# Optimization experiments

Measured on AMD Instinct MI355X. Metric: run time of the kernel, lower is better.

## Reference

```python
import jax, jax.numpy as jnp
import numpy as np

# ---- static module config (HashEncoder defaults) ----
INPUT_DIM = 3
NUM_LEVELS = 16
LEVEL_DIM = 2
PER_LEVEL_SCALE = 2.0
BASE_RES = 16
LOG2_HASHMAP = 19
MAX_PARAMS = 2 ** LOG2_HASHMAP
S = np.log2(PER_LEVEL_SCALE)  # log2 of per-level scale, as in the CUDA kernel
B_POINTS = 1048576

# per-level table offsets, exactly as in HashEncoder.__init__
_offs = [0]
_off = 0
for _i in range(NUM_LEVELS):
    _res = int(np.ceil(BASE_RES * PER_LEVEL_SCALE ** _i))
    _p = min(MAX_PARAMS, (_res + 1) ** INPUT_DIM)
    _p = int(_p / 8) * 8
    _off += _p
    _offs.append(_off)
OFFSETS = np.array(_offs, dtype=np.int64)
N_ENTRIES = _off  # 7132272

# spatial hash primes from torch-ngp fast_hash (first 3 dims)
PRIMES = np.array([1, 2654435761, 805459861], dtype=np.uint32)


def _encode_level(inputs, emb_level, level, hashmap_size):
    """One resolution level: hash 8 corners, gather, trilinear-interp. inputs: [B,3] in [0,1]."""
    scale = np.float32(np.exp2(level * S) * BASE_RES - 1.0)
    resolution = int(np.ceil(scale)) + 1
    pos = inputs * scale + 0.5
    pos_grid = jnp.floor(pos)
    frac = pos - pos_grid                    # [B,3] trilinear fractions
    pg = pos_grid.astype(jnp.uint32)         # [B,3] base corner
    # kernel hashes whenever the dense grid would exceed the (rounded) table size
    use_hash = (resolution + 1) ** INPUT_DIM > hashmap_size
    hs = np.uint32(hashmap_size)
    out = jnp.zeros((inputs.shape[0], LEVEL_DIM), dtype=inputs.dtype)
    for c in range(2 ** INPUT_DIM):          # 8 corners
        bits = np.array([(c >> d) & 1 for d in range(INPUT_DIM)], dtype=np.uint32)
        w = jnp.prod(jnp.where(bits.astype(bool), frac, 1.0 - frac), axis=-1)  # [B]
        corner = pg + bits                   # [B,3] uint32
        if use_hash:
            h = corner * PRIMES              # uint32 wrap-around multiply
            idx = h[:, 0] ^ h[:, 1] ^ h[:, 2]
        else:
            stride = np.uint32(resolution + 1)
            idx = corner[:, 0] + corner[:, 1] * stride + corner[:, 2] * (stride * stride)
        idx = (idx % hs).astype(jnp.int32)
        out = out + w[:, None] * emb_level[idx]  # irregular gather [B,C]
    return out


def setup_inputs() -> dict:
    key = jax.random.key(0)
    k1, k2 = jax.random.split(key)
    xyz = jax.random.uniform(k1, (B_POINTS, INPUT_DIM), dtype=jnp.float32)
    # reset_parameters: uniform(-1e-4, 1e-4)
    embeddings = jax.random.uniform(k2, (N_ENTRIES, LEVEL_DIM), dtype=jnp.float32,
                                    minval=-1e-4, maxval=1e-4)
    return {"xyz": xyz, "embeddings": embeddings, "normalize": 0}


def reference(xyz, embeddings, normalize):
    # normalize == 0 -> use raw coords (kernel expects [0,1]^3), matching normalize=False path
    inputs = xyz.reshape(-1, INPUT_DIM)
    outs = []
    for l in range(NUM_LEVELS):
        o0, o1 = int(OFFSETS[l]), int(OFFSETS[l + 1])
        outs.append(_encode_level(inputs, embeddings[o0:o1], l, o1 - o0))
    # equivalent to outputs.permute(1,0,2).reshape(B, L*C)
    return jnp.concatenate(outs, axis=-1)
```

## Files before the change

### kernel.cpp

```cpp
#include <hip/hip_runtime.h>

#define NLEVELS 16
#define BLOCK 256
#define PPT 2

struct HashParams {
    unsigned offs[NLEVELS + 1];
    unsigned hsize[NLEVELS];
    unsigned hash_bits;
    unsigned pow2_bits;
};

__global__ void __launch_bounds__(BLOCK)
hashenc_pass1(const float* __restrict__ xyz,
              const float* __restrict__ emb,
              float2* __restrict__ ws,
              HashParams p, int np, int bpl_shift)
{
    const int l = blockIdx.x >> bpl_shift;
    const int chunk = blockIdx.x & ((1 << bpl_shift) - 1);
    const int tid = threadIdx.x;

    const unsigned hs = p.hsize[l];
    const float2* __restrict__ tab = (const float2*)emb + p.offs[l];
    const float scale = (float)((16u << l) - 1u);
    const bool do_hash = (p.hash_bits >> l) & 1u;
    const bool is_pow2 = (p.pow2_bits >> l) & 1u;
    float2* __restrict__ wl = ws + (size_t)l * np;

    const int base = chunk * (BLOCK * PPT) + tid;

#pragma unroll
    for (int s = 0; s < PPT; ++s) {
        const int pidx = base + s * BLOCK;
        const float x = xyz[pidx * 3 + 0];
        const float y = xyz[pidx * 3 + 1];
        const float z = xyz[pidx * 3 + 2];

        const float px = x * scale + 0.5f;
        const float py = y * scale + 0.5f;
        const float pz = z * scale + 0.5f;
        const float gx = floorf(px), gy = floorf(py), gz = floorf(pz);
        const float fx = px - gx, fy = py - gy, fz = pz - gz;
        const unsigned ix = (unsigned)gx, iy = (unsigned)gy, iz = (unsigned)gz;

        unsigned idx[8];
        if (do_hash) {
            const unsigned hy0 = iy * 2654435761u;
            const unsigned hz0 = iz * 805459861u;
            const unsigned hy1 = hy0 + 2654435761u;
            const unsigned hz1 = hz0 + 805459861u;
            if (is_pow2) {
                const unsigned m = hs - 1u;
#pragma unroll
                for (int c = 0; c < 8; ++c)
                    idx[c] = ((ix + (c & 1)) ^ ((c & 2) ? hy1 : hy0) ^ ((c & 4) ? hz1 : hz0)) & m;
            } else {
#pragma unroll
                for (int c = 0; c < 8; ++c)
                    idx[c] = ((ix + (c & 1)) ^ ((c & 2) ? hy1 : hy0) ^ ((c & 4) ? hz1 : hz0)) % hs;
            }
        } else {
            const unsigned stride = (16u << l) + 1u;
#pragma unroll
            for (int c = 0; c < 8; ++c) {
                const unsigned lin = (ix + (c & 1))
                                   + (iy + ((c >> 1) & 1)) * stride
                                   + (iz + ((c >> 2) & 1)) * stride * stride;
                idx[c] = lin % hs;
            }
        }

        float2 e[8];
#pragma unroll
        for (int c = 0; c < 8; ++c) e[c] = tab[idx[c]];

        const float wx[2] = {1.0f - fx, fx};
        const float wy[2] = {1.0f - fy, fy};
        const float wz[2] = {1.0f - fz, fz};
        float o0 = 0.0f, o1 = 0.0f;
#pragma unroll
        for (int c = 0; c < 8; ++c) {
            const float w = wx[c & 1] * wy[(c >> 1) & 1] * wz[(c >> 2) & 1];
            o0 = fmaf(w, e[c].x, o0);
            o1 = fmaf(w, e[c].y, o1);
        }
        wl[pidx] = make_float2(o0, o1);
    }
}

__global__ void __launch_bounds__(BLOCK)
hashenc_pass2(const float2* __restrict__ ws, float* __restrict__ out, int np)
{
    __shared__ float lds[BLOCK * 33];
    const int tid = threadIdx.x;
    const int p0 = blockIdx.x * BLOCK;

#pragma unroll
    for (int l = 0; l < NLEVELS; ++l) {
        const float2 v = ws[(size_t)l * np + p0 + tid];
        lds[tid * 33 + 2 * l + 0] = v.x;
        lds[tid * 33 + 2 * l + 1] = v.y;
    }
    __syncthreads();
    float* __restrict__ ochunk = out + (size_t)blockIdx.x * (BLOCK * 32);
#pragma unroll
    for (int k = 0; k < 32; ++k) {
        const int flat = k * BLOCK + tid;
        const float v = lds[(flat >> 5) * 33 + (flat & 31)];
        __builtin_nontemporal_store(v, ochunk + flat);
    }
}

__global__ void __launch_bounds__(BLOCK)
hashenc_fwd(const float* __restrict__ xyz,
            const float* __restrict__ emb,
            float* __restrict__ out,
            HashParams p)
{
    const int tid = threadIdx.x;
    const long b = (long)blockIdx.x * BLOCK + tid;
    __shared__ float lds[BLOCK * 33];

    const float x = xyz[b * 3 + 0];
    const float y = xyz[b * 3 + 1];
    const float z = xyz[b * 3 + 2];

#pragma unroll
    for (int l = 0; l < NLEVELS; ++l) {
        const float scale = (float)((16u << l) - 1u);
        const float px = x * scale + 0.5f;
        const float py = y * scale + 0.5f;
        const float pz = z * scale + 0.5f;
        const float gx = floorf(px), gy = floorf(py), gz = floorf(pz);
        const float fx = px - gx, fy = py - gy, fz = pz - gz;
        const unsigned ix = (unsigned)gx, iy = (unsigned)gy, iz = (unsigned)gz;
        const unsigned hs = p.hsize[l];
        const float2* __restrict__ tab = (const float2*)emb + p.offs[l];

        unsigned idx[8];
        if ((p.hash_bits >> l) & 1u) {
            const unsigned hy0 = iy * 2654435761u;
            const unsigned hz0 = iz * 805459861u;
            const unsigned hy1 = hy0 + 2654435761u;
            const unsigned hz1 = hz0 + 805459861u;
            if ((p.pow2_bits >> l) & 1u) {
                const unsigned m = hs - 1u;
#pragma unroll
                for (int c = 0; c < 8; ++c)
                    idx[c] = ((ix + (c & 1)) ^ ((c & 2) ? hy1 : hy0) ^ ((c & 4) ? hz1 : hz0)) & m;
            } else {
#pragma unroll
                for (int c = 0; c < 8; ++c)
                    idx[c] = ((ix + (c & 1)) ^ ((c & 2) ? hy1 : hy0) ^ ((c & 4) ? hz1 : hz0)) % hs;
            }
        } else {
            const unsigned stride = (16u << l) + 1u;
#pragma unroll
            for (int c = 0; c < 8; ++c) {
                const unsigned lin = (ix + (c & 1))
                                   + (iy + ((c >> 1) & 1)) * stride
                                   + (iz + ((c >> 2) & 1)) * stride * stride;
                idx[c] = lin % hs;
            }
        }

        float2 e[8];
#pragma unroll
        for (int c = 0; c < 8; ++c) e[c] = tab[idx[c]];

        const float wx[2] = {1.0f - fx, fx};
        const float wy[2] = {1.0f - fy, fy};
        const float wz[2] = {1.0f - fz, fz};
        float o0 = 0.0f, o1 = 0.0f;
#pragma unroll
        for (int c = 0; c < 8; ++c) {
            const float w = wx[c & 1] * wy[(c >> 1) & 1] * wz[(c >> 2) & 1];
            o0 = fmaf(w, e[c].x, o0);
            o1 = fmaf(w, e[c].y, o1);
        }
        lds[tid * 33 + l * 2 + 0] = o0;
        lds[tid * 33 + l * 2 + 1] = o1;
    }

    __syncthreads();
    float* __restrict__ ochunk = out + (long)blockIdx.x * (BLOCK * 32);
#pragma unroll
    for (int k = 0; k < 32; ++k) {
        const int flat = k * BLOCK + tid;
        const float v = lds[(flat >> 5) * 33 + (flat & 31)];
        __builtin_nontemporal_store(v, ochunk + flat);
    }
}

extern "C" void kernel_launch(void* const* d_in, const int* in_sizes, int n_in,
                              void* d_out, int out_size, void* d_ws, size_t ws_size,
                              hipStream_t stream) {
    const float* xyz = (const float*)d_in[0];
    const float* emb = (const float*)d_in[1];
    float* out = (float*)d_out;
    const int B = in_sizes[0] / 3;

    HashParams p;
    p.offs[0] = 0;
    unsigned hash_bits = 0, pow2_bits = 0;
    long off = 0;
    for (int i = 0; i < NLEVELS; ++i) {
        const long res = 16L << i;
        const long dense = (res + 1) * (res + 1) * (res + 1);
        long t = dense < (1L << 19) ? dense : (1L << 19);
        t = (t / 8) * 8;
        p.hsize[i] = (unsigned)t;
        off += t;
        p.offs[i + 1] = (unsigned)off;
        if (dense > t) hash_bits |= (1u << i);
        if ((t & (t - 1)) == 0) pow2_bits |= (1u << i);
    }
    p.hash_bits = hash_bits;
    p.pow2_bits = pow2_bits;

    const size_t need = (size_t)B * NLEVELS * sizeof(float2);
    if (ws_size >= need && (B % (BLOCK * PPT)) == 0 && (B % BLOCK) == 0) {
        int bpl_shift = 0;
        while ((1 << bpl_shift) * (BLOCK * PPT) < B) ++bpl_shift;
        const int bpl = 1 << bpl_shift;
        hashenc_pass1<<<dim3(NLEVELS * bpl), dim3(BLOCK), 0, stream>>>(
            xyz, emb, (float2*)d_ws, p, B, bpl_shift);
        hashenc_pass2<<<dim3(B / BLOCK), dim3(BLOCK), 0, stream>>>(
            (const float2*)d_ws, out, B);
    } else {
        hashenc_fwd<<<dim3(B / BLOCK), dim3(BLOCK), 0, stream>>>(xyz, emb, out, p);
    }
}
```

Before: 594.3 us.

## Pair x-adjacent hash corners into float4 loads and block workspace layout

For power-of-two hashed levels, an even ix means the two x-neighbour corners hash to adjacent entries (index differs only in bit 0). The pass-1 kernel then fetches both with one 16-byte aligned load and swaps the halves by parity, cutting gather instructions from 8 to 4 for roughly half the points. The workspace is also reorganised into 256-point chunks holding all levels contiguously, so pass 2 reads one contiguous region per block. This adds branch divergence between the paired and unpaired paths inside each wavefront.

```diff
diff --git a/kernel.cpp b/kernel.cpp
--- a/kernel.cpp
+++ b/kernel.cpp
@@ -26,7 +26,6 @@
     const float scale = (float)((16u << l) - 1u);
     const bool do_hash = (p.hash_bits >> l) & 1u;
     const bool is_pow2 = (p.pow2_bits >> l) & 1u;
-    float2* __restrict__ wl = ws + (size_t)l * np;
 
     const int base = chunk * (BLOCK * PPT) + tid;
 
@@ -44,48 +43,86 @@
         const float fx = px - gx, fy = py - gy, fz = pz - gz;
         const unsigned ix = (unsigned)gx, iy = (unsigned)gy, iz = (unsigned)gz;
 
-        unsigned idx[8];
-        if (do_hash) {
+        const float wxv[2] = {1.0f - fx, fx};
+        const float wyv[2] = {1.0f - fy, fy};
+        const float wzv[2] = {1.0f - fz, fz};
+        float o0 = 0.0f, o1 = 0.0f;
+
+        if (do_hash && is_pow2) {
+            const unsigned m = hs - 1u;
             const unsigned hy0 = iy * 2654435761u;
             const unsigned hz0 = iz * 805459861u;
             const unsigned hy1 = hy0 + 2654435761u;
             const unsigned hz1 = hz0 + 805459861u;
-            if (is_pow2) {
-                const unsigned m = hs - 1u;
-#pragma unroll
-                for (int c = 0; c < 8; ++c)
-                    idx[c] = ((ix + (c & 1)) ^ ((c & 2) ? hy1 : hy0) ^ ((c & 4) ? hz1 : hz0)) & m;
+            const unsigned hyz[4] = { hy0 ^ hz0, hy1 ^ hz0, hy0 ^ hz1, hy1 ^ hz1 };
+
+            if (!(ix & 1u)) {
+                float4 pr[4];
+                unsigned vv[4];
+#pragma unroll
+                for (int q = 0; q < 4; ++q) {
+                    vv[q] = (ix ^ hyz[q]) & m;
+                    pr[q] = *reinterpret_cast<const float4*>(tab + (vv[q] & ~1u));
+                }
+#pragma unroll
+                for (int q = 0; q < 4; ++q) {
+                    const bool sw = (vv[q] & 1u) != 0u;
+                    const float ex0x = sw ? pr[q].z : pr[q].x;
+                    const float ex0y = sw ? pr[q].w : pr[q].y;
+                    const float ex1x = sw ? pr[q].x : pr[q].z;
+                    const float ex1y = sw ? pr[q].y : pr[q].w;
+                    const float w0 = wxv[0] * wyv[q & 1] * wzv[(q >> 1) & 1];
+                    const float w1 = wxv[1] * wyv[q & 1] * wzv[(q >> 1) & 1];
+                    o0 = fmaf(w0, ex0x, o0); o1 = fmaf(w0, ex0y, o1);
+                    o0 = fmaf(w1, ex1x, o0); o1 = fmaf(w1, ex1y, o1);
+                }
             } else {
+                float2 e0[4], e1[4];
+#pragma unroll
+                for (int q = 0; q < 4; ++q) {
+                    e0[q] = tab[(ix ^ hyz[q]) & m];
+                    e1[q] = tab[((ix + 1u) ^ hyz[q]) & m];
+                }
+#pragma unroll
+                for (int q = 0; q < 4; ++q) {
+                    const float w0 = wxv[0] * wyv[q & 1] * wzv[(q >> 1) & 1];
+                    const float w1 = wxv[1] * wyv[q & 1] * wzv[(q >> 1) & 1];
+                    o0 = fmaf(w0, e0[q].x, o0); o1 = fmaf(w0, e0[q].y, o1);
+                    o0 = fmaf(w1, e1[q].x, o0); o1 = fmaf(w1, e1[q].y, o1);
+                }
+            }
+        } else {
+            unsigned idx[8];
+            if (do_hash) {
+                const unsigned hy0 = iy * 2654435761u;
+                const unsigned hz0 = iz * 805459861u;
+                const unsigned hy1 = hy0 + 2654435761u;
+                const unsigned hz1 = hz0 + 805459861u;
 #pragma unroll
                 for (int c = 0; c < 8; ++c)
                     idx[c] = ((ix + (c & 1)) ^ ((c & 2) ? hy1 : hy0) ^ ((c & 4) ? hz1 : hz0)) % hs;
-            }
-        } else {
-            const unsigned stride = (16u << l) + 1u;
+            } else {
+                const unsigned stride = (16u << l) + 1u;
+#pragma unroll
+                for (int c = 0; c < 8; ++c) {
+                    const unsigned lin = (ix + (c & 1))
+                                       + (iy + ((c >> 1) & 1)) * stride
+                                       + (iz + ((c >> 2) & 1)) * stride * stride;
+                    idx[c] = lin % hs;
+                }
+            }
+            float2 e[8];
+#pragma unroll
+            for (int c = 0; c < 8; ++c) e[c] = tab[idx[c]];
 #pragma unroll
             for (int c = 0; c < 8; ++c) {
-                const unsigned lin = (ix + (c & 1))
-                                   + (iy + ((c >> 1) & 1)) * stride
-                                   + (iz + ((c >> 2) & 1)) * stride * stride;
-                idx[c] = lin % hs;
+                const float w = wxv[c & 1] * wyv[(c >> 1) & 1] * wzv[(c >> 2) & 1];
+                o0 = fmaf(w, e[c].x, o0);
+                o1 = fmaf(w, e[c].y, o1);
             }
         }
 
-        float2 e[8];
-#pragma unroll
-        for (int c = 0; c < 8; ++c) e[c] = tab[idx[c]];
-
-        const float wx[2] = {1.0f - fx, fx};
-        const float wy[2] = {1.0f - fy, fy};
-        const float wz[2] = {1.0f - fz, fz};
-        float o0 = 0.0f, o1 = 0.0f;
-#pragma unroll
-        for (int c = 0; c < 8; ++c) {
-            const float w = wx[c & 1] * wy[(c >> 1) & 1] * wz[(c >> 2) & 1];
-            o0 = fmaf(w, e[c].x, o0);
-            o1 = fmaf(w, e[c].y, o1);
-        }
-        wl[pidx] = make_float2(o0, o1);
+        ws[((size_t)(pidx >> 8) * NLEVELS + l) * 256 + (pidx & 255)] = make_float2(o0, o1);
     }
 }
 
@@ -94,11 +131,11 @@
 {
     __shared__ float lds[BLOCK * 33];
     const int tid = threadIdx.x;
-    const int p0 = blockIdx.x * BLOCK;
+    const float2* __restrict__ chunk = ws + (size_t)blockIdx.x * (NLEVELS * 256);
 
 #pragma unroll
     for (int l = 0; l < NLEVELS; ++l) {
-        const float2 v = ws[(size_t)l * np + p0 + tid];
+        const float2 v = chunk[l * 256 + tid];
         lds[tid * 33 + 2 * l + 0] = v.x;
         lds[tid * 33 + 2 * l + 1] = v.y;
     }
@@ -220,13 +257,13 @@
     p.pow2_bits = pow2_bits;
 
     const size_t need = (size_t)B * NLEVELS * sizeof(float2);
-    if (ws_size >= need && (B % (BLOCK * PPT)) == 0 && (B % BLOCK) == 0) {
+    if (ws_size >= need && (B % (BLOCK * PPT)) == 0 && (B % 256) == 0) {
         int bpl_shift = 0;
         while ((1 << bpl_shift) * (BLOCK * PPT) < B) ++bpl_shift;
         const int bpl = 1 << bpl_shift;
         hashenc_pass1<<<dim3(NLEVELS * bpl), dim3(BLOCK), 0, stream>>>(
             xyz, emb, (float2*)d_ws, p, B, bpl_shift);
-        hashenc_pass2<<<dim3(B / BLOCK), dim3(BLOCK), 0, stream>>>(
+        hashenc_pass2<<<dim3(B / 256), dim3(BLOCK), 0, stream>>>(
             (const float2*)d_ws, out, B);
     } else {
         hashenc_fwd<<<dim3(B / BLOCK), dim3(BLOCK), 0, stream>>>(xyz, emb, out, p);
```

Measured after the change: 572.5 us. 3.7% less time.

## Convert embedding table to fp16 and pair x-neighbour corner gathers

Applied to the files above, without the earlier changes.

Each call first runs a conversion kernel that packs the float32 embedding table into half2 entries in workspace. The per-level pass then gathers these 4-byte entries, and when the x coordinate is even it fetches the two x-neighbour corners with a single 8-byte load, choosing their order from the low bit of the hash. The dense levels drop the modulo in favour of a conditional subtract, and xyz is staged through LDS with float4 loads. The aim is to halve gather bytes and gather count; the cost is an extra pass over the table every call and fp16 rounding of the embeddings.

```diff
diff --git a/kernel.cpp b/kernel.cpp
--- a/kernel.cpp
+++ b/kernel.cpp
@@ -1,4 +1,5 @@
 #include <hip/hip_runtime.h>
+#include <hip/hip_fp16.h>
 
 #define NLEVELS 16
 #define BLOCK 256
@@ -12,14 +13,147 @@
 };
 
 __global__ void __launch_bounds__(BLOCK)
-hashenc_pass1(const float* __restrict__ xyz,
-              const float* __restrict__ emb,
-              float2* __restrict__ ws,
-              HashParams p, int np, int bpl_shift)
+hashenc_conv(const float4* __restrict__ emb2, uint2* __restrict__ tab16, int n2)
+{
+    const int i = blockIdx.x * BLOCK + threadIdx.x;
+    if (i < n2) {
+        const float4 v = emb2[i];
+        const __half2 a = __floats2half2_rn(v.x, v.y);
+        const __half2 b = __floats2half2_rn(v.z, v.w);
+        tab16[i] = make_uint2(*(const unsigned*)&a, *(const unsigned*)&b);
+    }
+}
+
+__global__ void __launch_bounds__(BLOCK)
+hashenc_pass1_h(const float* __restrict__ xyz,
+                const unsigned* __restrict__ tab16,
+                float2* __restrict__ ws,
+                HashParams p, int np, int bpl_shift)
 {
     const int l = blockIdx.x >> bpl_shift;
     const int chunk = blockIdx.x & ((1 << bpl_shift) - 1);
     const int tid = threadIdx.x;
+
+    __shared__ float sxyz[BLOCK * PPT * 3];
+    {
+        const float4* __restrict__ src =
+            (const float4*)(xyz + (size_t)chunk * (BLOCK * PPT) * 3);
+        float4* __restrict__ dst = (float4*)sxyz;
+#pragma unroll
+        for (int i = tid; i < (BLOCK * PPT * 3) / 4; i += BLOCK)
+            dst[i] = src[i];
+    }
+    __syncthreads();
+
+    const unsigned hs = p.hsize[l];
+    const unsigned* __restrict__ tab = tab16 + p.offs[l];
+    const float scale = (float)((16u << l) - 1u);
+    const bool do_hash = (p.hash_bits >> l) & 1u;
+    float2* __restrict__ wl = ws + (size_t)l * np;
+
+    unsigned raw[PPT][8];
+    unsigned selba[PPT];
+    float fxa[PPT], fya[PPT], fza[PPT];
+
+#pragma unroll
+    for (int s = 0; s < PPT; ++s) {
+        const int lp = s * BLOCK + tid;
+        const float x = sxyz[lp * 3 + 0];
+        const float y = sxyz[lp * 3 + 1];
+        const float z = sxyz[lp * 3 + 2];
+        const float px = x * scale + 0.5f;
+        const float py = y * scale + 0.5f;
+        const float pz = z * scale + 0.5f;
+        const float gx = floorf(px), gy = floorf(py), gz = floorf(pz);
+        fxa[s] = px - gx; fya[s] = py - gy; fza[s] = pz - gz;
+        const unsigned ix = (unsigned)gx, iy = (unsigned)gy, iz = (unsigned)gz;
+
+        unsigned selb = 0u;
+        if (do_hash) {
+            const unsigned m = hs - 1u;
+            const unsigned hy0 = iy * 2654435761u;
+            const unsigned hz0 = iz * 805459861u;
+            const unsigned hy1 = hy0 + 2654435761u;
+            const unsigned hz1 = hz0 + 805459861u;
+            const unsigned hyz[4] = { hy0 ^ hz0, hy1 ^ hz0, hy0 ^ hz1, hy1 ^ hz1 };
+            if (!(ix & 1u)) {
+#pragma unroll
+                for (int q = 0; q < 4; ++q) {
+                    const unsigned v0 = (ix ^ hyz[q]) & m;
+                    const uint2 pr = *reinterpret_cast<const uint2*>(tab + (v0 & ~1u));
+                    raw[s][2 * q]     = pr.x;
+                    raw[s][2 * q + 1] = pr.y;
+                    selb |= (v0 & 1u) << q;
+                }
+            } else {
+#pragma unroll
+                for (int q = 0; q < 4; ++q) {
+                    raw[s][2 * q]     = tab[(ix ^ hyz[q]) & m];
+                    raw[s][2 * q + 1] = tab[((ix + 1u) ^ hyz[q]) & m];
+                }
+            }
+        } else {
+            const unsigned stride = (16u << l) + 1u;
+#pragma unroll
+            for (int q = 0; q < 4; ++q) {
+                const unsigned base = ix + (iy + (q & 1u)) * stride
+                                         + (iz + (unsigned)(q >> 1)) * stride * stride;
+                const unsigned l0 = base, l1 = base + 1u;
+                const unsigned v0 = l0 - (l0 >= hs ? hs : 0u);
+                const unsigned v1 = l1 - (l1 >= hs ? hs : 0u);
+                raw[s][2 * q]     = tab[v0];
+                raw[s][2 * q + 1] = tab[v1];
+            }
+        }
+        selba[s] = selb;
+    }
+
+#pragma unroll
+    for (int s = 0; s < PPT; ++s) {
+        const float fx = fxa[s], fy = fya[s], fz = fza[s];
+        const float wxv[2] = {1.0f - fx, fx};
+        const float wyv[2] = {1.0f - fy, fy};
+        const float wzv[2] = {1.0f - fz, fz};
+        const unsigned selb = selba[s];
+        float o0 = 0.0f, o1 = 0.0f;
+#pragma unroll
+        for (int q = 0; q < 4; ++q) {
+            const unsigned r0 = raw[s][2 * q], r1 = raw[s][2 * q + 1];
+            const bool sw = (selb >> q) & 1u;
+            const unsigned ua = sw ? r1 : r0;
+            const unsigned ub = sw ? r0 : r1;
+            const float2 ea = __half22float2(*reinterpret_cast<const __half2*>(&ua));
+            const float2 eb = __half22float2(*reinterpret_cast<const __half2*>(&ub));
+            const float wq = wyv[q & 1] * wzv[q >> 1];
+            const float w0 = wxv[0] * wq, w1 = wxv[1] * wq;
+            o0 = fmaf(w0, ea.x, o0); o1 = fmaf(w0, ea.y, o1);
+            o0 = fmaf(w1, eb.x, o0); o1 = fmaf(w1, eb.y, o1);
+        }
+        const int pidx = chunk * (BLOCK * PPT) + s * BLOCK + tid;
+        wl[pidx] = make_float2(o0, o1);
+    }
+}
+
+__global__ void __launch_bounds__(BLOCK)
+hashenc_pass1_f32(const float* __restrict__ xyz,
+                  const float* __restrict__ emb,
+                  float2* __restrict__ ws,
+                  HashParams p, int np, int bpl_shift)
+{
+    const int l = blockIdx.x >> bpl_shift;
+    const int chunk = blockIdx.x & ((1 << bpl_shift) - 1);
+    const int tid = threadIdx.x;
+
+    __shared__ float sxyz[BLOCK * PPT * 3];
+    {
+        const float4* __restrict__ src =
+            (const float4*)(xyz + (size_t)chunk * (BLOCK * PPT) * 3);
+        float4* __restrict__ dst = (float4*)sxyz;
+#pragma unroll
+        for (int i = tid; i < (BLOCK * PPT * 3) / 4; i += BLOCK)
+            dst[i] = src[i];
+    }
+    __syncthreads();
 
     const unsigned hs = p.hsize[l];
     const float2* __restrict__ tab = (const float2*)emb + p.offs[l];
@@ -28,22 +162,23 @@
     const bool is_pow2 = (p.pow2_bits >> l) & 1u;
     float2* __restrict__ wl = ws + (size_t)l * np;
 
-    const int base = chunk * (BLOCK * PPT) + tid;
-
 #pragma unroll
     for (int s = 0; s < PPT; ++s) {
-        const int pidx = base + s * BLOCK;
-        const float x = xyz[pidx * 3 + 0];
-        const float y = xyz[pidx * 3 + 1];
-        const float z = xyz[pidx * 3 + 2];
-
+        const int lp = s * BLOCK + tid;
+        const int pidx = chunk * (BLOCK * PPT) + lp;
+        const float x = sxyz[lp * 3 + 0];
+        const float y = sxyz[lp * 3 + 1];
+        const float z = sxyz[lp * 3 + 2];
         const float px = x * scale + 0.5f;
         const float py = y * scale + 0.5f;
         const float pz = z * scale + 0.5f;
         const float gx = floorf(px), gy = floorf(py), gz = floorf(pz);
         const float fx = px - gx, fy = py - gy, fz = pz - gz;
         const unsigned ix = (unsigned)gx, iy = (unsigned)gy, iz = (unsigned)gz;
-
+        const float wxv[2] = {1.0f - fx, fx};
+        const float wyv[2] = {1.0f - fy, fy};
+        const float wzv[2] = {1.0f - fz, fz};
+        float o0 = 0.0f, o1 = 0.0f;
         unsigned idx[8];
         if (do_hash) {
             const unsigned hy0 = iy * 2654435761u;
@@ -70,18 +205,12 @@
                 idx[c] = lin % hs;
             }
         }
-
         float2 e[8];
 #pragma unroll
         for (int c = 0; c < 8; ++c) e[c] = tab[idx[c]];
-
-        const float wx[2] = {1.0f - fx, fx};
-        const float wy[2] = {1.0f - fy, fy};
-        const float wz[2] = {1.0f - fz, fz};
-        float o0 = 0.0f, o1 = 0.0f;
 #pragma unroll
         for (int c = 0; c < 8; ++c) {
-            const float w = wx[c & 1] * wy[(c >> 1) & 1] * wz[(c >> 2) & 1];
+            const float w = wxv[c & 1] * wyv[(c >> 1) & 1] * wzv[(c >> 2) & 1];
             o0 = fmaf(w, e[c].x, o0);
             o1 = fmaf(w, e[c].y, o1);
         }
@@ -219,12 +348,29 @@
     p.hash_bits = hash_bits;
     p.pow2_bits = pow2_bits;
 
+    const long nent = off;
     const size_t need = (size_t)B * NLEVELS * sizeof(float2);
-    if (ws_size >= need && (B % (BLOCK * PPT)) == 0 && (B % BLOCK) == 0) {
+    const size_t need_h = need + (size_t)nent * 4;
+    const bool shape_ok = (B % (BLOCK * PPT)) == 0 && (B % BLOCK) == 0;
+    const bool hashed_all_pow2 = (hash_bits & ~pow2_bits) == 0;
+
+    if (shape_ok && hashed_all_pow2 && ws_size >= need_h) {
+        unsigned* tab16 = (unsigned*)((char*)d_ws + need);
+        const int n2 = (int)(nent / 2);
+        hashenc_conv<<<dim3((n2 + BLOCK - 1) / BLOCK), dim3(BLOCK), 0, stream>>>(
+            (const float4*)emb, (uint2*)tab16, n2);
         int bpl_shift = 0;
         while ((1 << bpl_shift) * (BLOCK * PPT) < B) ++bpl_shift;
         const int bpl = 1 << bpl_shift;
-        hashenc_pass1<<<dim3(NLEVELS * bpl), dim3(BLOCK), 0, stream>>>(
+        hashenc_pass1_h<<<dim3(NLEVELS * bpl), dim3(BLOCK), 0, stream>>>(
+            xyz, tab16, (float2*)d_ws, p, B, bpl_shift);
+        hashenc_pass2<<<dim3(B / BLOCK), dim3(BLOCK), 0, stream>>>(
+            (const float2*)d_ws, out, B);
+    } else if (shape_ok && ws_size >= need) {
+        int bpl_shift = 0;
+        while ((1 << bpl_shift) * (BLOCK * PPT) < B) ++bpl_shift;
+        const int bpl = 1 << bpl_shift;
+        hashenc_pass1_f32<<<dim3(NLEVELS * bpl), dim3(BLOCK), 0, stream>>>(
             xyz, emb, (float2*)d_ws, p, B, bpl_shift);
         hashenc_pass2<<<dim3(B / BLOCK), dim3(BLOCK), 0, stream>>>(
             (const float2*)d_ws, out, B);
```

Result: no change. 583.3 us (-1.9%).
